# Optimization experiments

Hardware: AMD Instinct MI355X
Metric: run time of the kernel (lower is better)

## Reference

```python
import jax, jax.numpy as jnp
import numpy as np

# dims
B, T, F, R, H = 2048, 50, 64, 6, 64      # batch, time, features, num_rims, hidden per rim
KS, VS = 64, 128                          # input attention key/query size, value size
NC, QC, VC = 4, 32, 16                    # comm heads, comm key/query size, comm value (NC*VC == H)
S = 16                                    # static features
K_ACT = 4                                 # active rims (top-k routing)


def setup_inputs() -> dict:
    key = jax.random.key(0)
    ks = jax.random.split(key, 24)
    f32 = jnp.float32
    rn = lambda k, shape, scale: jax.random.normal(k, shape, f32) * scale
    inp = {}
    inp['x'] = jax.random.normal(ks[0], (B, T, F), f32)
    inp['statics'] = jax.random.normal(ks[1], (B, S), f32)
    inp['mask'] = (jax.random.uniform(ks[2], (B, T, F)) > 0.3).astype(f32)
    inp['delta'] = jax.random.uniform(ks[3], (B, T, F), f32) * 5.0
    inp['x_last_observed'] = jax.random.normal(ks[4], (B, T, F), f32)
    inp['x_mean'] = jax.random.normal(ks[5], (B, F), f32)
    # GRU-D style per-feature input decay params
    inp['w_dg'] = rn(ks[6], (F,), 0.1)
    inp['b_dg'] = jnp.zeros((F,), f32)
    # input attention (shared K/V over the 2-slot [input, null] axis; per-rim group query)
    inp['Wk'] = rn(ks[7], (F, KS), 1.0 / np.sqrt(F))
    inp['Wv'] = rn(ks[8], (F, VS), 1.0 / np.sqrt(F))
    inp['Wq'] = rn(ks[9], (R, H, KS), 1.0 / np.sqrt(H))
    # per-rim (group) GRU cell
    inp['W_ih'] = rn(ks[10], (R, VS, 3 * H), 1.0 / np.sqrt(VS))
    inp['W_hh'] = rn(ks[11], (R, H, 3 * H), 1.0 / np.sqrt(H))
    inp['b_ih'] = jnp.zeros((R, 3 * H), f32)
    inp['b_hh'] = jnp.zeros((R, 3 * H), f32)
    # communication attention (per-rim group projections)
    inp['Wq_c'] = rn(ks[12], (R, H, NC * QC), 1.0 / np.sqrt(H))
    inp['Wk_c'] = rn(ks[13], (R, H, NC * QC), 1.0 / np.sqrt(H))
    inp['Wv_c'] = rn(ks[14], (R, H, NC * VC), 1.0 / np.sqrt(H))
    # MLP head
    inp['W1'] = rn(ks[15], (R * H + S, 10), 1.0 / np.sqrt(R * H + S))
    inp['b1'] = jnp.zeros((10,), f32)
    inp['W2'] = rn(ks[16], (10, 2), 1.0 / np.sqrt(10))
    inp['b2'] = jnp.zeros((2,), f32)
    return inp


def reference(x, statics, mask, delta, x_last_observed, x_mean,
              w_dg, b_dg, Wk, Wv, Wq, W_ih, W_hh, b_ih, b_hh,
              Wq_c, Wk_c, Wv_c, W1, b1, W2, b2):
    Bn = x.shape[0]
    inv_sk = 1.0 / np.sqrt(KS).astype(np.float32)
    inv_sq = 1.0 / np.sqrt(QC).astype(np.float32)

    def step(h, inp_t):
        xt, mt, dt, xlt = inp_t  # each [B,F]
        # GRU-D input decay / imputation
        gamma = jnp.exp(-jax.nn.relu(dt * w_dg + b_dg))
        xh = mt * xt + (1.0 - mt) * (gamma * xlt + (1.0 - gamma) * x_mean)
        # input attention over [real, null] slots
        x_in = jnp.stack([xh, jnp.zeros_like(xh)], axis=1)          # [B,2,F]
        Km = x_in @ Wk                                               # [B,2,KS]
        Vm = x_in @ Wv                                               # [B,2,VS]
        Q = jnp.einsum('brh,rhk->brk', h, Wq)                        # [B,R,KS]
        probs = jax.nn.softmax(jnp.einsum('brk,bnk->brn', Q, Km) * inv_sk, axis=-1)  # [B,R,2]
        inputs = jnp.einsum('brn,bnv->brv', probs, Vm)               # [B,R,VS]
        # top-k active rims = least attention to the null slot
        act_idx = jax.lax.top_k(-probs[:, :, 1], K_ACT)[1]           # [B,K_ACT]
        rim_mask = jnp.sum(jax.nn.one_hot(act_idx, R, dtype=h.dtype), axis=1)  # [B,R]
        # per-rim GRU update (blocked GEMMs)
        gi = jnp.einsum('brv,rvg->brg', inputs, W_ih) + b_ih         # [B,R,3H]
        gh = jnp.einsum('brh,rhg->brg', h, W_hh) + b_hh              # [B,R,3H]
        i_r, i_z, i_n = jnp.split(gi, 3, axis=-1)
        h_r, h_z, h_n = jnp.split(gh, 3, axis=-1)
        r = jax.nn.sigmoid(i_r + h_r)
        z = jax.nn.sigmoid(i_z + h_z)
        n = jnp.tanh(i_n + r * h_n)
        h_new = (1.0 - z) * n + z * h                                # [B,R,H]
        # communication attention among rims
        q = jnp.einsum('brh,rhk->brk', h_new, Wq_c).reshape(Bn, R, NC, QC).transpose(0, 2, 1, 3)
        k = jnp.einsum('brh,rhk->brk', h_new, Wk_c).reshape(Bn, R, NC, QC).transpose(0, 2, 1, 3)
        v = jnp.einsum('brh,rhk->brk', h_new, Wv_c).reshape(Bn, R, NC, VC).transpose(0, 2, 1, 3)
        cprobs = jax.nn.softmax(jnp.einsum('bcrk,bcsk->bcrs', q, k) * inv_sq, axis=-1)  # [B,NC,R,R]
        comm = jnp.einsum('bcrs,bcsv->bcrv', cprobs, v).transpose(0, 2, 1, 3).reshape(Bn, R, NC * VC)
        # only active rims are updated (and receive comm); inactive keep old state
        m = rim_mask[..., None]
        h_out = m * (h_new + comm) + (1.0 - m) * h
        return h_out, None

    h0 = jnp.zeros((Bn, R, H), x.dtype)
    seq = (x.transpose(1, 0, 2), mask.transpose(1, 0, 2),
           delta.transpose(1, 0, 2), x_last_observed.transpose(1, 0, 2))
    hT, _ = jax.lax.scan(step, h0, seq)
    full = jnp.concatenate([hT.reshape(Bn, R * H), statics], axis=1)
    predictions = jax.nn.relu(full @ W1 + b1) @ W2 + b2              # [B,2]
    return predictions
```

## Files before the change

### kernel.cpp

```cpp
#include <hip/hip_runtime.h>
#include <math.h>

#define B_TOT 2048
#define T_STEPS 50
#define F_DIM 64
#define R_RIMS 6
#define H_DIM 64
#define K_ACT 4
#define BB 8

__device__ __forceinline__ void fma4(float4& a, const float4 v, const float s) {
  a.x = fmaf(v.x, s, a.x); a.y = fmaf(v.y, s, a.y);
  a.z = fmaf(v.z, s, a.z); a.w = fmaf(v.w, s, a.w);
}
__device__ __forceinline__ float sigmoidf_(float x) { return 1.0f / (1.0f + __expf(-x)); }
__device__ __forceinline__ float tanhf_(float x) {
  float ax = fabsf(x);
  float e = __expf(-2.0f * ax);
  float t = (1.0f - e) / (1.0f + e);
  return copysignf(t, x);
}

__global__ void wcomb_kernel(const float* __restrict__ Wv, const float* __restrict__ Wih,
                             float* __restrict__ Wc) {
  int g = threadIdx.x;
  int f = blockIdx.x & 63;
  int r = blockIdx.x >> 6;
  float acc = 0.f;
#pragma unroll 8
  for (int v = 0; v < 128; ++v)
    acc = fmaf(Wv[f * 128 + v], Wih[(r * 128 + v) * 192 + g], acc);
  Wc[(r * 64 + f) * 192 + g] = acc;
}

__global__ __launch_bounds__(512, 1) void rims_kernel(
    const float* __restrict__ x, const float* __restrict__ statics,
    const float* __restrict__ maskp, const float* __restrict__ delta,
    const float* __restrict__ xlast, const float* __restrict__ xmean,
    const float* __restrict__ wdgp, const float* __restrict__ bdgp,
    const float* __restrict__ Wk, const float* __restrict__ Wq,
    const float* __restrict__ Whh, const float* __restrict__ bih,
    const float* __restrict__ bhh, const float* __restrict__ Wqc,
    const float* __restrict__ Wkc, const float* __restrict__ Wvc,
    const float* __restrict__ W1, const float* __restrict__ b1,
    const float* __restrict__ W2, const float* __restrict__ b2,
    const float* __restrict__ Wcomb, float* __restrict__ out) {
  __shared__ float xh_T[64][8];
  __shared__ float h_T[6][64][8];
  __shared__ float hn_T[6][64][8];
  __shared__ float K0_T[64][9];
  __shared__ float Q_T[6][64][9];
  __shared__ float qc_T[6][128][9];
  __shared__ float kc_T[6][128][9];
  __shared__ float vc_T[6][64][9];
  __shared__ float bih_l[6 * 192];
  __shared__ float bhh_l[6 * 192];
  __shared__ float p0_l[8][6];
  __shared__ float act_l[8][6];

  const int tid = threadIdx.x;
  const int wave = tid >> 6;
  const int lane = tid & 63;
  const int b0 = blockIdx.x * BB;

  for (int i = tid; i < 6 * 192; i += 512) { bih_l[i] = bih[i]; bhh_l[i] = bhh[i]; }
  for (int i = tid; i < 6 * 64 * 8; i += 512) (&h_T[0][0][0])[i] = 0.f;

  const float wdg = wdgp[lane];
  const float bdg = bdgp[lane];
  const float xmv = xmean[(size_t)(b0 + wave) * 64 + lane];
  __syncthreads();

  for (int t = 0; t < T_STEPS; ++t) {
    {
      size_t off = ((size_t)(b0 + wave) * T_STEPS + t) * 64 + lane;
      float xt = x[off], mt = maskp[off], dt = delta[off], xl = xlast[off];
      float gm = __expf(-fmaxf(fmaf(dt, wdg, bdg), 0.f));
      xh_T[lane][wave] = mt * xt + (1.f - mt) * (gm * xl + (1.f - gm) * xmv);
    }
    __syncthreads();
    if (wave < 7) {
      const float* Ws = (wave == 0) ? Wk : (Wq + (wave - 1) * 64 * 64);
      const float(*src)[8] = (wave == 0) ? xh_T : h_T[wave - 1];
      float4 aL = {0, 0, 0, 0}, aH = {0, 0, 0, 0};
#pragma unroll 8
      for (int l2 = 0; l2 < 64; ++l2) {
        float w = Ws[l2 * 64 + lane];
        float4 sa = *(const float4*)&src[l2][0];
        float4 sb = *(const float4*)&src[l2][4];
        fma4(aL, sa, w); fma4(aH, sb, w);
      }
      float* dst = (wave == 0) ? &K0_T[lane][0] : &Q_T[wave - 1][lane][0];
      dst[0] = aL.x; dst[1] = aL.y; dst[2] = aL.z; dst[3] = aL.w;
      dst[4] = aH.x; dst[5] = aH.y; dst[6] = aH.z; dst[7] = aH.w;
    }
    __syncthreads();
    {
      float k0 = K0_T[lane][wave];
      float logit[6];
#pragma unroll
      for (int r = 0; r < 6; ++r) {
        float p = Q_T[r][lane][wave] * k0;
#pragma unroll
        for (int d = 1; d < 64; d <<= 1) p += __shfl_xor(p, d, 64);
        logit[r] = p * 0.125f;
      }
      if (lane == 0) {
#pragma unroll
        for (int r = 0; r < 6; ++r) {
          int rank = 0;
#pragma unroll
          for (int r2 = 0; r2 < 6; ++r2)
            rank += (logit[r2] > logit[r]) || (logit[r2] == logit[r] && r2 < r);
          p0_l[wave][r] = sigmoidf_(logit[r]);
          act_l[wave][r] = (rank < K_ACT) ? 1.f : 0.f;
        }
      }
    }
    __syncthreads();
    if (wave < 6) {
      const int r = wave;
      const float* Wc = Wcomb + r * 64 * 192;
      const float* Wh = Whh + r * 64 * 192;
      float4 uaL = {0,0,0,0}, uaH = {0,0,0,0}, ubL = {0,0,0,0}, ubH = {0,0,0,0},
             ucL = {0,0,0,0}, ucH = {0,0,0,0};
      float4 gaL = {0,0,0,0}, gaH = {0,0,0,0}, gbL = {0,0,0,0}, gbH = {0,0,0,0},
             gcL = {0,0,0,0}, gcH = {0,0,0,0};
#pragma unroll 4
      for (int l2 = 0; l2 < 64; ++l2) {
        const float* wr = Wc + l2 * 192 + lane;
        float w0 = wr[0], w1 = wr[64], w2 = wr[128];
        const float* vr = Wh + l2 * 192 + lane;
        float v0 = vr[0], v1 = vr[64], v2 = vr[128];
        float4 xa = *(const float4*)&xh_T[l2][0];
        float4 xb = *(const float4*)&xh_T[l2][4];
        float4 ha = *(const float4*)&h_T[r][l2][0];
        float4 hb = *(const float4*)&h_T[r][l2][4];
        fma4(uaL, xa, w0); fma4(uaH, xb, w0);
        fma4(ubL, xa, w1); fma4(ubH, xb, w1);
        fma4(ucL, xa, w2); fma4(ucH, xb, w2);
        fma4(gaL, ha, v0); fma4(gaH, hb, v0);
        fma4(gbL, ha, v1); fma4(gbH, hb, v1);
        fma4(gcL, ha, v2); fma4(gcH, hb, v2);
      }
      const float bir = bih_l[r * 192 + lane], biz = bih_l[r * 192 + 64 + lane],
                  bin = bih_l[r * 192 + 128 + lane];
      const float bhr = bhh_l[r * 192 + lane], bhz = bhh_l[r * 192 + 64 + lane],
                  bhn = bhh_l[r * 192 + 128 + lane];
      float4 holdL = *(const float4*)&h_T[r][lane][0];
      float4 holdH = *(const float4*)&h_T[r][lane][4];
      auto gru1 = [&](float p0v, float u0, float u1, float u2, float g0, float g1,
                      float g2, float hold) -> float {
        float rg = sigmoidf_(fmaf(p0v, u0, bir) + g0 + bhr);
        float zg = sigmoidf_(fmaf(p0v, u1, biz) + g1 + bhz);
        float ng = tanhf_(fmaf(p0v, u2, bin) + rg * (g2 + bhn));
        return (1.f - zg) * ng + zg * hold;
      };
      float4 hnL, hnH;
      hnL.x = gru1(p0_l[0][r], uaL.x, ubL.x, ucL.x, gaL.x, gbL.x, gcL.x, holdL.x);
      hnL.y = gru1(p0_l[1][r], uaL.y, ubL.y, ucL.y, gaL.y, gbL.y, gcL.y, holdL.y);
      hnL.z = gru1(p0_l[2][r], uaL.z, ubL.z, ucL.z, gaL.z, gbL.z, gcL.z, holdL.z);
      hnL.w = gru1(p0_l[3][r], uaL.w, ubL.w, ucL.w, gaL.w, gbL.w, gcL.w, holdL.w);
      hnH.x = gru1(p0_l[4][r], uaH.x, ubH.x, ucH.x, gaH.x, gbH.x, gcH.x, holdH.x);
      hnH.y = gru1(p0_l[5][r], uaH.y, ubH.y, ucH.y, gaH.y, gbH.y, gcH.y, holdH.y);
      hnH.z = gru1(p0_l[6][r], uaH.z, ubH.z, ucH.z, gaH.z, gbH.z, gcH.z, holdH.z);
      hnH.w = gru1(p0_l[7][r], uaH.w, ubH.w, ucH.w, gaH.w, gbH.w, gcH.w, holdH.w);
      *(float4*)&hn_T[r][lane][0] = hnL;
      *(float4*)&hn_T[r][lane][4] = hnH;
    }
    __syncthreads();
    for (int uu = wave; uu < 15; uu += 8) {
      if (uu < 12) {
        const int r = (uu < 6) ? uu : (uu - 6);
        const float* Ws = ((uu < 6) ? Wqc : Wkc) + r * 64 * 128;
        float4 a0L = {0,0,0,0}, a0H = {0,0,0,0}, a1L = {0,0,0,0}, a1H = {0,0,0,0};
#pragma unroll 4
        for (int l2 = 0; l2 < 64; ++l2) {
          float w0 = Ws[l2 * 128 + lane], w1 = Ws[l2 * 128 + 64 + lane];
          float4 ha = *(const float4*)&hn_T[r][l2][0];
          float4 hb = *(const float4*)&hn_T[r][l2][4];
          fma4(a0L, ha, w0); fma4(a0H, hb, w0);
          fma4(a1L, ha, w1); fma4(a1H, hb, w1);
        }
        float(*dst)[9] = (uu < 6) ? qc_T[r] : kc_T[r];
        float* d0 = &dst[lane][0];
        d0[0] = a0L.x; d0[1] = a0L.y; d0[2] = a0L.z; d0[3] = a0L.w;
        d0[4] = a0H.x; d0[5] = a0H.y; d0[6] = a0H.z; d0[7] = a0H.w;
        float* d1 = &dst[lane + 64][0];
        d1[0] = a1L.x; d1[1] = a1L.y; d1[2] = a1L.z; d1[3] = a1L.w;
        d1[4] = a1H.x; d1[5] = a1H.y; d1[6] = a1H.z; d1[7] = a1H.w;
      } else {
        const int rA = (uu - 12) * 2, rB = rA + 1;
        float4 a0L = {0,0,0,0}, a0H = {0,0,0,0}, a1L = {0,0,0,0}, a1H = {0,0,0,0};
#pragma unroll 4
        for (int l2 = 0; l2 < 64; ++l2) {
          float w0 = Wvc[(rA * 64 + l2) * 64 + lane];
          float w1 = Wvc[(rB * 64 + l2) * 64 + lane];
          float4 ha = *(const float4*)&hn_T[rA][l2][0];
          float4 hb = *(const float4*)&hn_T[rA][l2][4];
          float4 hc = *(const float4*)&hn_T[rB][l2][0];
          float4 hd = *(const float4*)&hn_T[rB][l2][4];
          fma4(a0L, ha, w0); fma4(a0H, hb, w0);
          fma4(a1L, hc, w1); fma4(a1H, hd, w1);
        }
        float* d0 = &vc_T[rA][lane][0];
        d0[0] = a0L.x; d0[1] = a0L.y; d0[2] = a0L.z; d0[3] = a0L.w;
        d0[4] = a0H.x; d0[5] = a0H.y; d0[6] = a0H.z; d0[7] = a0H.w;
        float* d1 = &vc_T[rB][lane][0];
        d1[0] = a1L.x; d1[1] = a1L.y; d1[2] = a1L.z; d1[3] = a1L.w;
        d1[4] = a1H.x; d1[5] = a1H.y; d1[6] = a1H.z; d1[7] = a1H.w;
      }
    }
    __syncthreads();
    {
      const int bb = wave;
      float qcA[6], qcB[6], kcA[6], kcB[6], vcv[6];
#pragma unroll
      for (int rr = 0; rr < 6; ++rr) {
        qcA[rr] = qc_T[rr][lane][bb]; qcB[rr] = qc_T[rr][lane + 64][bb];
        kcA[rr] = kc_T[rr][lane][bb]; kcB[rr] = kc_T[rr][lane + 64][bb];
        vcv[rr] = vc_T[rr][lane][bb];
      }
      const int cOut = lane >> 4;
      const int srcLane = (cOut & 1) << 5;
      const float inv_sq = 0.17677669529663687f;
#pragma unroll
      for (int rr = 0; rr < 6; ++rr) {
        float sL[6], sH[6];
#pragma unroll
        for (int s = 0; s < 6; ++s) {
          float p = qcA[rr] * kcA[s];
          p += __shfl_xor(p, 1, 64); p += __shfl_xor(p, 2, 64); p += __shfl_xor(p, 4, 64);
          p += __shfl_xor(p, 8, 64); p += __shfl_xor(p, 16, 64);
          sL[s] = p * inv_sq;
          float q = qcB[rr] * kcB[s];
          q += __shfl_xor(q, 1, 64); q += __shfl_xor(q, 2, 64); q += __shfl_xor(q, 4, 64);
          q += __shfl_xor(q, 8, 64); q += __shfl_xor(q, 16, 64);
          sH[s] = q * inv_sq;
        }
        float mL = sL[0], mH = sH[0];
#pragma unroll
        for (int s = 1; s < 6; ++s) { mL = fmaxf(mL, sL[s]); mH = fmaxf(mH, sH[s]); }
        float sumL = 0.f, sumH = 0.f;
#pragma unroll
        for (int s = 0; s < 6; ++s) {
          sL[s] = __expf(sL[s] - mL); sumL += sL[s];
          sH[s] = __expf(sH[s] - mH); sumH += sH[s];
        }
        float rLn = 1.f / sumL, rHn = 1.f / sumH;
        float comm = 0.f;
#pragma unroll
        for (int s = 0; s < 6; ++s) {
          float tL = __shfl(sL[s] * rLn, srcLane, 64);
          float tH = __shfl(sH[s] * rHn, srcLane, 64);
          float cp = (cOut < 2) ? tL : tH;
          comm = fmaf(cp, vcv[s], comm);
        }
        float mk = act_l[bb][rr];
        float hnv = hn_T[rr][lane][bb];
        float hov = h_T[rr][lane][bb];
        h_T[rr][lane][bb] = (mk > 0.5f) ? (hnv + comm) : hov;
      }
    }
    __syncthreads();
  }

  {
    const int b = b0 + wave;
    float acc[10];
#pragma unroll
    for (int o = 0; o < 10; ++o) acc[o] = 0.f;
#pragma unroll
    for (int ii = 0; ii < 6; ++ii) {
      float f = h_T[ii][lane][wave];
      const float* w = W1 + (ii * 64 + lane) * 10;
#pragma unroll
      for (int o = 0; o < 10; ++o) acc[o] = fmaf(f, w[o], acc[o]);
    }
    if (lane < 16) {
      float f = statics[(size_t)b * 16 + lane];
      const float* w = W1 + (384 + lane) * 10;
#pragma unroll
      for (int o = 0; o < 10; ++o) acc[o] = fmaf(f, w[o], acc[o]);
    }
#pragma unroll
    for (int o = 0; o < 10; ++o) {
#pragma unroll
      for (int d = 1; d < 64; d <<= 1) acc[o] += __shfl_xor(acc[o], d, 64);
    }
    if (lane == 0) {
      float o0 = b2[0], o1 = b2[1];
#pragma unroll
      for (int o = 0; o < 10; ++o) {
        float a = fmaxf(acc[o] + b1[o], 0.f);
        o0 = fmaf(a, W2[o * 2 + 0], o0);
        o1 = fmaf(a, W2[o * 2 + 1], o1);
      }
      out[(size_t)b * 2 + 0] = o0;
      out[(size_t)b * 2 + 1] = o1;
    }
  }
}

extern "C" void kernel_launch(void* const* d_in, const int* in_sizes, int n_in,
                              void* d_out, int out_size, void* d_ws, size_t ws_size,
                              hipStream_t stream) {
  const float* x       = (const float*)d_in[0];
  const float* statics = (const float*)d_in[1];
  const float* maskp   = (const float*)d_in[2];
  const float* delta   = (const float*)d_in[3];
  const float* xlast   = (const float*)d_in[4];
  const float* xmean   = (const float*)d_in[5];
  const float* wdg     = (const float*)d_in[6];
  const float* bdg     = (const float*)d_in[7];
  const float* Wk      = (const float*)d_in[8];
  const float* Wv      = (const float*)d_in[9];
  const float* Wq      = (const float*)d_in[10];
  const float* Wih     = (const float*)d_in[11];
  const float* Whh     = (const float*)d_in[12];
  const float* bih     = (const float*)d_in[13];
  const float* bhh     = (const float*)d_in[14];
  const float* Wqc     = (const float*)d_in[15];
  const float* Wkc     = (const float*)d_in[16];
  const float* Wvc     = (const float*)d_in[17];
  const float* W1      = (const float*)d_in[18];
  const float* b1      = (const float*)d_in[19];
  const float* W2      = (const float*)d_in[20];
  const float* b2      = (const float*)d_in[21];
  float* Wcomb = (float*)d_ws;

  wcomb_kernel<<<384, 192, 0, stream>>>(Wv, Wih, Wcomb);
  rims_kernel<<<256, 512, 0, stream>>>(x, statics, maskp, delta, xlast, xmean,
                                       wdg, bdg, Wk, Wq, Whh, bih, bhh,
                                       Wqc, Wkc, Wvc, W1, b1, W2, b2,
                                       Wcomb, (float*)d_out);
}
```

Measured before the change: 1.737 ms.

## Halve per-block batch, transpose weights for float4 loads, raise occupancy

```diff
diff --git a/kernel.cpp b/kernel.cpp
--- a/kernel.cpp
+++ b/kernel.cpp
@@ -1,13 +1,16 @@
 #include <hip/hip_runtime.h>
 #include <math.h>
 
-#define B_TOT 2048
 #define T_STEPS 50
-#define F_DIM 64
-#define R_RIMS 6
-#define H_DIM 64
-#define K_ACT 4
-#define BB 8
+#define BB 4
+
+#define OFF_WCT   0
+#define OFF_WHHT  73728
+#define OFF_WQT   147456
+#define OFF_WKT   172032
+#define OFF_WQCT  176128
+#define OFF_WKCT  225280
+#define OFF_WVCT  274432
 
 __device__ __forceinline__ void fma4(float4& a, const float4 v, const float s) {
   a.x = fmaf(v.x, s, a.x); a.y = fmaf(v.y, s, a.y);
@@ -21,58 +24,86 @@
   return copysignf(t, x);
 }
 
-__global__ void wcomb_kernel(const float* __restrict__ Wv, const float* __restrict__ Wih,
-                             float* __restrict__ Wc) {
-  int g = threadIdx.x;
-  int f = blockIdx.x & 63;
-  int r = blockIdx.x >> 6;
+__global__ void wcombT_kernel(const float* __restrict__ Wv, const float* __restrict__ Wih,
+                              float* __restrict__ ws) {
+  int f = threadIdx.x;
+  int g = blockIdx.x % 192;
+  int r = blockIdx.x / 192;
   float acc = 0.f;
 #pragma unroll 8
   for (int v = 0; v < 128; ++v)
     acc = fmaf(Wv[f * 128 + v], Wih[(r * 128 + v) * 192 + g], acc);
-  Wc[(r * 64 + f) * 192 + g] = acc;
-}
-
-__global__ __launch_bounds__(512, 1) void rims_kernel(
+  ws[OFF_WCT + (r * 192 + g) * 64 + f] = acc;
+}
+
+__global__ void prep_transpose(const float* __restrict__ Whh, const float* __restrict__ Wq,
+                               const float* __restrict__ Wk, const float* __restrict__ Wqc,
+                               const float* __restrict__ Wkc, const float* __restrict__ Wvc,
+                               float* __restrict__ ws) {
+  int i = blockIdx.x * 256 + threadIdx.x;
+  if (i < 73728) {
+    int r = i / 12288, rem = i % 12288, g = rem / 64, h2 = rem % 64;
+    ws[OFF_WHHT + i] = Whh[(r * 64 + h2) * 192 + g];
+  } else if (i < 98304) {
+    int j = i - 73728;
+    int r = j / 4096, rem = j % 4096, k = rem / 64, h2 = rem % 64;
+    ws[OFF_WQT + j] = Wq[(r * 64 + h2) * 64 + k];
+  } else if (i < 102400) {
+    int j = i - 98304;
+    int k = j / 64, f = j % 64;
+    ws[OFF_WKT + j] = Wk[f * 64 + k];
+  } else if (i < 151552) {
+    int j = i - 102400;
+    int r = j / 8192, rem = j % 8192, g = rem / 64, h2 = rem % 64;
+    ws[OFF_WQCT + j] = Wqc[(r * 64 + h2) * 128 + g];
+  } else if (i < 200704) {
+    int j = i - 151552;
+    int r = j / 8192, rem = j % 8192, g = rem / 64, h2 = rem % 64;
+    ws[OFF_WKCT + j] = Wkc[(r * 64 + h2) * 128 + g];
+  } else if (i < 225280) {
+    int j = i - 200704;
+    int r = j / 4096, rem = j % 4096, g = rem / 64, h2 = rem % 64;
+    ws[OFF_WVCT + j] = Wvc[(r * 64 + h2) * 64 + g];
+  }
+}
+
+__global__ __launch_bounds__(512, 4) void rims_kernel(
     const float* __restrict__ x, const float* __restrict__ statics,
     const float* __restrict__ maskp, const float* __restrict__ delta,
     const float* __restrict__ xlast, const float* __restrict__ xmean,
     const float* __restrict__ wdgp, const float* __restrict__ bdgp,
-    const float* __restrict__ Wk, const float* __restrict__ Wq,
-    const float* __restrict__ Whh, const float* __restrict__ bih,
-    const float* __restrict__ bhh, const float* __restrict__ Wqc,
-    const float* __restrict__ Wkc, const float* __restrict__ Wvc,
+    const float* __restrict__ bih, const float* __restrict__ bhh,
     const float* __restrict__ W1, const float* __restrict__ b1,
     const float* __restrict__ W2, const float* __restrict__ b2,
-    const float* __restrict__ Wcomb, float* __restrict__ out) {
-  __shared__ float xh_T[64][8];
-  __shared__ float h_T[6][64][8];
-  __shared__ float hn_T[6][64][8];
-  __shared__ float K0_T[64][9];
-  __shared__ float Q_T[6][64][9];
-  __shared__ float qc_T[6][128][9];
-  __shared__ float kc_T[6][128][9];
-  __shared__ float vc_T[6][64][9];
-  __shared__ float bih_l[6 * 192];
-  __shared__ float bhh_l[6 * 192];
-  __shared__ float p0_l[8][6];
-  __shared__ float act_l[8][6];
+    const float* __restrict__ ws, float* __restrict__ out) {
+  __shared__ float xh_T[64][4];
+  __shared__ float h_T[6][64][4];
+  __shared__ float hn_T[6][64][4];
+  __shared__ float K0_R[4][64];
+  __shared__ float Q_R[6][4][64];
+  __shared__ float qc_R[6][4][128];
+  __shared__ float kc_R[6][4][128];
+  __shared__ float vc_R[6][4][64];
+  __shared__ float bih_l[1152];
+  __shared__ float bhh_l[1152];
+  __shared__ float p0_l[4][6];
+  __shared__ float act_l[4][6];
 
   const int tid = threadIdx.x;
   const int wave = tid >> 6;
   const int lane = tid & 63;
   const int b0 = blockIdx.x * BB;
 
-  for (int i = tid; i < 6 * 192; i += 512) { bih_l[i] = bih[i]; bhh_l[i] = bhh[i]; }
-  for (int i = tid; i < 6 * 64 * 8; i += 512) (&h_T[0][0][0])[i] = 0.f;
+  for (int i = tid; i < 1152; i += 512) { bih_l[i] = bih[i]; bhh_l[i] = bhh[i]; }
+  for (int i = tid; i < 6 * 64 * 4; i += 512) (&h_T[0][0][0])[i] = 0.f;
 
   const float wdg = wdgp[lane];
   const float bdg = bdgp[lane];
-  const float xmv = xmean[(size_t)(b0 + wave) * 64 + lane];
+  const float xmv = xmean[(size_t)(b0 + (wave & 3)) * 64 + lane];
   __syncthreads();
 
   for (int t = 0; t < T_STEPS; ++t) {
-    {
+    if (wave < 4) {
       size_t off = ((size_t)(b0 + wave) * T_STEPS + t) * 64 + lane;
       float xt = x[off], mt = maskp[off], dt = delta[off], xl = xlast[off];
       float gm = __expf(-fmaxf(fmaf(dt, wdg, bdg), 0.f));
@@ -80,27 +111,34 @@
     }
     __syncthreads();
     if (wave < 7) {
-      const float* Ws = (wave == 0) ? Wk : (Wq + (wave - 1) * 64 * 64);
-      const float(*src)[8] = (wave == 0) ? xh_T : h_T[wave - 1];
-      float4 aL = {0, 0, 0, 0}, aH = {0, 0, 0, 0};
-#pragma unroll 8
-      for (int l2 = 0; l2 < 64; ++l2) {
-        float w = Ws[l2 * 64 + lane];
-        float4 sa = *(const float4*)&src[l2][0];
-        float4 sb = *(const float4*)&src[l2][4];
-        fma4(aL, sa, w); fma4(aH, sb, w);
-      }
-      float* dst = (wave == 0) ? &K0_T[lane][0] : &Q_T[wave - 1][lane][0];
-      dst[0] = aL.x; dst[1] = aL.y; dst[2] = aL.z; dst[3] = aL.w;
-      dst[4] = aH.x; dst[5] = aH.y; dst[6] = aH.z; dst[7] = aH.w;
-    }
-    __syncthreads();
-    {
-      float k0 = K0_T[lane][wave];
+      const float* WT = (wave == 0) ? (ws + OFF_WKT) : (ws + OFF_WQT + (wave - 1) * 4096);
+      const float(*srcT)[4] = (wave == 0) ? xh_T : h_T[wave - 1];
+      float4 acc = {0, 0, 0, 0};
+#pragma unroll 4
+      for (int kk = 0; kk < 16; ++kk) {
+        float4 wv = *(const float4*)(WT + lane * 64 + kk * 4);
+        float4 a0 = *(const float4*)&srcT[kk * 4 + 0][0];
+        float4 a1 = *(const float4*)&srcT[kk * 4 + 1][0];
+        float4 a2 = *(const float4*)&srcT[kk * 4 + 2][0];
+        float4 a3 = *(const float4*)&srcT[kk * 4 + 3][0];
+        fma4(acc, a0, wv.x); fma4(acc, a1, wv.y); fma4(acc, a2, wv.z); fma4(acc, a3, wv.w);
+      }
+      if (wave == 0) {
+        K0_R[0][lane] = acc.x; K0_R[1][lane] = acc.y;
+        K0_R[2][lane] = acc.z; K0_R[3][lane] = acc.w;
+      } else {
+        float* q = &Q_R[wave - 1][0][0];
+        q[lane] = acc.x; q[64 + lane] = acc.y; q[128 + lane] = acc.z; q[192 + lane] = acc.w;
+      }
+    }
+    __syncthreads();
+    if (wave < 4) {
+      const int bb = wave;
+      float k0 = K0_R[bb][lane];
       float logit[6];
 #pragma unroll
       for (int r = 0; r < 6; ++r) {
-        float p = Q_T[r][lane][wave] * k0;
+        float p = Q_R[r][bb][lane] * k0;
 #pragma unroll
         for (int d = 1; d < 64; d <<= 1) p += __shfl_xor(p, d, 64);
         logit[r] = p * 0.125f;
@@ -112,128 +150,130 @@
 #pragma unroll
           for (int r2 = 0; r2 < 6; ++r2)
             rank += (logit[r2] > logit[r]) || (logit[r2] == logit[r] && r2 < r);
-          p0_l[wave][r] = sigmoidf_(logit[r]);
-          act_l[wave][r] = (rank < K_ACT) ? 1.f : 0.f;
+          p0_l[bb][r] = sigmoidf_(logit[r]);
+          act_l[bb][r] = (rank < 4) ? 1.f : 0.f;
         }
       }
     }
     __syncthreads();
     if (wave < 6) {
       const int r = wave;
-      const float* Wc = Wcomb + r * 64 * 192;
-      const float* Wh = Whh + r * 64 * 192;
-      float4 uaL = {0,0,0,0}, uaH = {0,0,0,0}, ubL = {0,0,0,0}, ubH = {0,0,0,0},
-             ucL = {0,0,0,0}, ucH = {0,0,0,0};
-      float4 gaL = {0,0,0,0}, gaH = {0,0,0,0}, gbL = {0,0,0,0}, gbH = {0,0,0,0},
-             gcL = {0,0,0,0}, gcH = {0,0,0,0};
-#pragma unroll 4
-      for (int l2 = 0; l2 < 64; ++l2) {
-        const float* wr = Wc + l2 * 192 + lane;
-        float w0 = wr[0], w1 = wr[64], w2 = wr[128];
-        const float* vr = Wh + l2 * 192 + lane;
-        float v0 = vr[0], v1 = vr[64], v2 = vr[128];
-        float4 xa = *(const float4*)&xh_T[l2][0];
-        float4 xb = *(const float4*)&xh_T[l2][4];
-        float4 ha = *(const float4*)&h_T[r][l2][0];
-        float4 hb = *(const float4*)&h_T[r][l2][4];
-        fma4(uaL, xa, w0); fma4(uaH, xb, w0);
-        fma4(ubL, xa, w1); fma4(ubH, xb, w1);
-        fma4(ucL, xa, w2); fma4(ucH, xb, w2);
-        fma4(gaL, ha, v0); fma4(gaH, hb, v0);
-        fma4(gbL, ha, v1); fma4(gbH, hb, v1);
-        fma4(gcL, ha, v2); fma4(gcH, hb, v2);
+      const float* WcT = ws + OFF_WCT + r * 12288;
+      const float* WhT = ws + OFF_WHHT + r * 12288;
+      float4 ua = {0,0,0,0}, ub = {0,0,0,0}, uc = {0,0,0,0};
+      float4 ga = {0,0,0,0}, gb = {0,0,0,0}, gc = {0,0,0,0};
+#pragma unroll 2
+      for (int kk = 0; kk < 16; ++kk) {
+        float4 w0 = *(const float4*)(WcT + lane * 64 + kk * 4);
+        float4 w1 = *(const float4*)(WcT + (lane + 64) * 64 + kk * 4);
+        float4 w2 = *(const float4*)(WcT + (lane + 128) * 64 + kk * 4);
+        float4 v0 = *(const float4*)(WhT + lane * 64 + kk * 4);
+        float4 v1 = *(const float4*)(WhT + (lane + 64) * 64 + kk * 4);
+        float4 v2 = *(const float4*)(WhT + (lane + 128) * 64 + kk * 4);
+#define G1J(J, W0C, W1C, W2C, V0C, V1C, V2C)                      \
+        {                                                          \
+          float4 xv = *(const float4*)&xh_T[kk * 4 + J][0];        \
+          float4 hv = *(const float4*)&h_T[r][kk * 4 + J][0];      \
+          fma4(ua, xv, W0C); fma4(ub, xv, W1C); fma4(uc, xv, W2C); \
+          fma4(ga, hv, V0C); fma4(gb, hv, V1C); fma4(gc, hv, V2C); \
+        }
+        G1J(0, w0.x, w1.x, w2.x, v0.x, v1.x, v2.x)
+        G1J(1, w0.y, w1.y, w2.y, v0.y, v1.y, v2.y)
+        G1J(2, w0.z, w1.z, w2.z, v0.z, v1.z, v2.z)
+        G1J(3, w0.w, w1.w, w2.w, v0.w, v1.w, v2.w)
+#undef G1J
       }
       const float bir = bih_l[r * 192 + lane], biz = bih_l[r * 192 + 64 + lane],
                   bin = bih_l[r * 192 + 128 + lane];
       const float bhr = bhh_l[r * 192 + lane], bhz = bhh_l[r * 192 + 64 + lane],
                   bhn = bhh_l[r * 192 + 128 + lane];
-      float4 holdL = *(const float4*)&h_T[r][lane][0];
-      float4 holdH = *(const float4*)&h_T[r][lane][4];
+      float4 hold = *(const float4*)&h_T[r][lane][0];
       auto gru1 = [&](float p0v, float u0, float u1, float u2, float g0, float g1,
-                      float g2, float hold) -> float {
+                      float g2, float holdv) -> float {
         float rg = sigmoidf_(fmaf(p0v, u0, bir) + g0 + bhr);
         float zg = sigmoidf_(fmaf(p0v, u1, biz) + g1 + bhz);
         float ng = tanhf_(fmaf(p0v, u2, bin) + rg * (g2 + bhn));
-        return (1.f - zg) * ng + zg * hold;
+        return (1.f - zg) * ng + zg * holdv;
       };
-      float4 hnL, hnH;
-      hnL.x = gru1(p0_l[0][r], uaL.x, ubL.x, ucL.x, gaL.x, gbL.x, gcL.x, holdL.x);
-      hnL.y = gru1(p0_l[1][r], uaL.y, ubL.y, ucL.y, gaL.y, gbL.y, gcL.y, holdL.y);
-      hnL.z = gru1(p0_l[2][r], uaL.z, ubL.z, ucL.z, gaL.z, gbL.z, gcL.z, holdL.z);
-      hnL.w = gru1(p0_l[3][r], uaL.w, ubL.w, ucL.w, gaL.w, gbL.w, gcL.w, holdL.w);
-      hnH.x = gru1(p0_l[4][r], uaH.x, ubH.x, ucH.x, gaH.x, gbH.x, gcH.x, holdH.x);
-      hnH.y = gru1(p0_l[5][r], uaH.y, ubH.y, ucH.y, gaH.y, gbH.y, gcH.y, holdH.y);
-      hnH.z = gru1(p0_l[6][r], uaH.z, ubH.z, ucH.z, gaH.z, gbH.z, gcH.z, holdH.z);
-      hnH.w = gru1(p0_l[7][r], uaH.w, ubH.w, ucH.w, gaH.w, gbH.w, gcH.w, holdH.w);
-      *(float4*)&hn_T[r][lane][0] = hnL;
-      *(float4*)&hn_T[r][lane][4] = hnH;
+      float4 hn;
+      hn.x = gru1(p0_l[0][r], ua.x, ub.x, uc.x, ga.x, gb.x, gc.x, hold.x);
+      hn.y = gru1(p0_l[1][r], ua.y, ub.y, uc.y, ga.y, gb.y, gc.y, hold.y);
+      hn.z = gru1(p0_l[2][r], ua.z, ub.z, uc.z, ga.z, gb.z, gc.z, hold.z);
+      hn.w = gru1(p0_l[3][r], ua.w, ub.w, uc.w, ga.w, gb.w, gc.w, hold.w);
+      *(float4*)&hn_T[r][lane][0] = hn;
     }
     __syncthreads();
     for (int uu = wave; uu < 15; uu += 8) {
       if (uu < 12) {
         const int r = (uu < 6) ? uu : (uu - 6);
-        const float* Ws = ((uu < 6) ? Wqc : Wkc) + r * 64 * 128;
-        float4 a0L = {0,0,0,0}, a0H = {0,0,0,0}, a1L = {0,0,0,0}, a1H = {0,0,0,0};
+        const float* WT = ws + ((uu < 6) ? OFF_WQCT : OFF_WKCT) + r * 8192;
+        float4 a0 = {0,0,0,0}, a1 = {0,0,0,0};
 #pragma unroll 4
-        for (int l2 = 0; l2 < 64; ++l2) {
-          float w0 = Ws[l2 * 128 + lane], w1 = Ws[l2 * 128 + 64 + lane];
-          float4 ha = *(const float4*)&hn_T[r][l2][0];
-          float4 hb = *(const float4*)&hn_T[r][l2][4];
-          fma4(a0L, ha, w0); fma4(a0H, hb, w0);
-          fma4(a1L, ha, w1); fma4(a1H, hb, w1);
-        }
-        float(*dst)[9] = (uu < 6) ? qc_T[r] : kc_T[r];
-        float* d0 = &dst[lane][0];
-        d0[0] = a0L.x; d0[1] = a0L.y; d0[2] = a0L.z; d0[3] = a0L.w;
-        d0[4] = a0H.x; d0[5] = a0H.y; d0[6] = a0H.z; d0[7] = a0H.w;
-        float* d1 = &dst[lane + 64][0];
-        d1[0] = a1L.x; d1[1] = a1L.y; d1[2] = a1L.z; d1[3] = a1L.w;
-        d1[4] = a1H.x; d1[5] = a1H.y; d1[6] = a1H.z; d1[7] = a1H.w;
+        for (int kk = 0; kk < 16; ++kk) {
+          float4 w0 = *(const float4*)(WT + lane * 64 + kk * 4);
+          float4 w1 = *(const float4*)(WT + (lane + 64) * 64 + kk * 4);
+#define C1J(J, W0C, W1C)                                      \
+          {                                                    \
+            float4 xv = *(const float4*)&hn_T[r][kk * 4 + J][0]; \
+            fma4(a0, xv, W0C); fma4(a1, xv, W1C);              \
+          }
+          C1J(0, w0.x, w1.x) C1J(1, w0.y, w1.y) C1J(2, w0.z, w1.z) C1J(3, w0.w, w1.w)
+#undef C1J
+        }
+        float* dst = (uu < 6) ? &qc_R[r][0][0] : &kc_R[r][0][0];
+        dst[0 * 128 + lane] = a0.x; dst[1 * 128 + lane] = a0.y;
+        dst[2 * 128 + lane] = a0.z; dst[3 * 128 + lane] = a0.w;
+        dst[0 * 128 + 64 + lane] = a1.x; dst[1 * 128 + 64 + lane] = a1.y;
+        dst[2 * 128 + 64 + lane] = a1.z; dst[3 * 128 + 64 + lane] = a1.w;
       } else {
         const int rA = (uu - 12) * 2, rB = rA + 1;
-        float4 a0L = {0,0,0,0}, a0H = {0,0,0,0}, a1L = {0,0,0,0}, a1H = {0,0,0,0};
+        const float* WT = ws + OFF_WVCT;
+        float4 a0 = {0,0,0,0}, a1 = {0,0,0,0};
 #pragma unroll 4
-        for (int l2 = 0; l2 < 64; ++l2) {
-          float w0 = Wvc[(rA * 64 + l2) * 64 + lane];
-          float w1 = Wvc[(rB * 64 + l2) * 64 + lane];
-          float4 ha = *(const float4*)&hn_T[rA][l2][0];
-          float4 hb = *(const float4*)&hn_T[rA][l2][4];
-          float4 hc = *(const float4*)&hn_T[rB][l2][0];
-          float4 hd = *(const float4*)&hn_T[rB][l2][4];
-          fma4(a0L, ha, w0); fma4(a0H, hb, w0);
-          fma4(a1L, hc, w1); fma4(a1H, hd, w1);
-        }
-        float* d0 = &vc_T[rA][lane][0];
-        d0[0] = a0L.x; d0[1] = a0L.y; d0[2] = a0L.z; d0[3] = a0L.w;
-        d0[4] = a0H.x; d0[5] = a0H.y; d0[6] = a0H.z; d0[7] = a0H.w;
-        float* d1 = &vc_T[rB][lane][0];
-        d1[0] = a1L.x; d1[1] = a1L.y; d1[2] = a1L.z; d1[3] = a1L.w;
-        d1[4] = a1H.x; d1[5] = a1H.y; d1[6] = a1H.z; d1[7] = a1H.w;
+        for (int kk = 0; kk < 16; ++kk) {
+          float4 w0 = *(const float4*)(WT + (rA * 64 + lane) * 64 + kk * 4);
+          float4 w1 = *(const float4*)(WT + (rB * 64 + lane) * 64 + kk * 4);
+#define C1V(J, W0C, W1C)                                        \
+          {                                                      \
+            float4 xa = *(const float4*)&hn_T[rA][kk * 4 + J][0]; \
+            float4 xb = *(const float4*)&hn_T[rB][kk * 4 + J][0]; \
+            fma4(a0, xa, W0C); fma4(a1, xb, W1C);                \
+          }
+          C1V(0, w0.x, w1.x) C1V(1, w0.y, w1.y) C1V(2, w0.z, w1.z) C1V(3, w0.w, w1.w)
+#undef C1V
+        }
+        vc_R[rA][0][lane] = a0.x; vc_R[rA][1][lane] = a0.y;
+        vc_R[rA][2][lane] = a0.z; vc_R[rA][3][lane] = a0.w;
+        vc_R[rB][0][lane] = a1.x; vc_R[rB][1][lane] = a1.y;
+        vc_R[rB][2][lane] = a1.z; vc_R[rB][3][lane] = a1.w;
       }
     }
     __syncthreads();
     {
-      const int bb = wave;
-      float qcA[6], qcB[6], kcA[6], kcB[6], vcv[6];
-#pragma unroll
-      for (int rr = 0; rr < 6; ++rr) {
-        qcA[rr] = qc_T[rr][lane][bb]; qcB[rr] = qc_T[rr][lane + 64][bb];
-        kcA[rr] = kc_T[rr][lane][bb]; kcB[rr] = kc_T[rr][lane + 64][bb];
-        vcv[rr] = vc_T[rr][lane][bb];
+      const int bb = wave >> 1;
+      const int half = wave & 1;
+      float kcA[6], kcB[6], vcv[6];
+#pragma unroll
+      for (int s = 0; s < 6; ++s) {
+        kcA[s] = kc_R[s][bb][lane];
+        kcB[s] = kc_R[s][bb][64 + lane];
+        vcv[s] = vc_R[s][bb][lane];
       }
       const int cOut = lane >> 4;
       const int srcLane = (cOut & 1) << 5;
       const float inv_sq = 0.17677669529663687f;
 #pragma unroll
-      for (int rr = 0; rr < 6; ++rr) {
+      for (int jr = 0; jr < 3; ++jr) {
+        const int rr = half * 3 + jr;
+        float qA = qc_R[rr][bb][lane], qB = qc_R[rr][bb][64 + lane];
         float sL[6], sH[6];
 #pragma unroll
         for (int s = 0; s < 6; ++s) {
-          float p = qcA[rr] * kcA[s];
+          float p = qA * kcA[s];
           p += __shfl_xor(p, 1, 64); p += __shfl_xor(p, 2, 64); p += __shfl_xor(p, 4, 64);
           p += __shfl_xor(p, 8, 64); p += __shfl_xor(p, 16, 64);
           sL[s] = p * inv_sq;
-          float q = qcB[rr] * kcB[s];
+          float q = qB * kcB[s];
           q += __shfl_xor(q, 1, 64); q += __shfl_xor(q, 2, 64); q += __shfl_xor(q, 4, 64);
           q += __shfl_xor(q, 8, 64); q += __shfl_xor(q, 16, 64);
           sH[s] = q * inv_sq;
@@ -265,7 +305,7 @@
     __syncthreads();
   }
 
-  {
+  if (wave < 4) {
     const int b = b0 + wave;
     float acc[10];
 #pragma unroll
@@ -327,11 +367,11 @@
   const float* b1      = (const float*)d_in[19];
   const float* W2      = (const float*)d_in[20];
   const float* b2      = (const float*)d_in[21];
-  float* Wcomb = (float*)d_ws;
-
-  wcomb_kernel<<<384, 192, 0, stream>>>(Wv, Wih, Wcomb);
-  rims_kernel<<<256, 512, 0, stream>>>(x, statics, maskp, delta, xlast, xmean,
-                                       wdg, bdg, Wk, Wq, Whh, bih, bhh,
-                                       Wqc, Wkc, Wvc, W1, b1, W2, b2,
-                                       Wcomb, (float*)d_out);
-}
+  float* ws = (float*)d_ws;
+
+  wcombT_kernel<<<1152, 64, 0, stream>>>(Wv, Wih, ws);
+  prep_transpose<<<880, 256, 0, stream>>>(Whh, Wq, Wk, Wqc, Wkc, Wvc, ws);
+  rims_kernel<<<512, 512, 0, stream>>>(x, statics, maskp, delta, xlast, xmean,
+                                       wdg, bdg, bih, bhh, W1, b1, W2, b2,
+                                       ws, (float*)d_out);
+}
```

After: 4.036 ms. +132.4%, slower.

## Double block to 1024 threads, splitting batch rows across wave pairs per stage

Applied to the files above, without the earlier changes.

```diff
diff --git a/kernel.cpp b/kernel.cpp
--- a/kernel.cpp
+++ b/kernel.cpp
@@ -1,12 +1,7 @@
 #include <hip/hip_runtime.h>
 #include <math.h>
 
-#define B_TOT 2048
 #define T_STEPS 50
-#define F_DIM 64
-#define R_RIMS 6
-#define H_DIM 64
-#define K_ACT 4
 #define BB 8
 
 __device__ __forceinline__ void fma4(float4& a, const float4 v, const float s) {
@@ -33,7 +28,7 @@
   Wc[(r * 64 + f) * 192 + g] = acc;
 }
 
-__global__ __launch_bounds__(512, 1) void rims_kernel(
+__global__ __launch_bounds__(1024, 1) void rims_kernel(
     const float* __restrict__ x, const float* __restrict__ statics,
     const float* __restrict__ maskp, const float* __restrict__ delta,
     const float* __restrict__ xlast, const float* __restrict__ xmean,
@@ -48,13 +43,11 @@
   __shared__ float xh_T[64][8];
   __shared__ float h_T[6][64][8];
   __shared__ float hn_T[6][64][8];
-  __shared__ float K0_T[64][9];
-  __shared__ float Q_T[6][64][9];
-  __shared__ float qc_T[6][128][9];
-  __shared__ float kc_T[6][128][9];
-  __shared__ float vc_T[6][64][9];
-  __shared__ float bih_l[6 * 192];
-  __shared__ float bhh_l[6 * 192];
+  __shared__ float K0_R[8][64];
+  __shared__ float Q_R[6][8][64];
+  __shared__ float qc_R[6][8][128];
+  __shared__ float kc_R[6][8][128];
+  __shared__ float vc_R[6][8][64];
   __shared__ float p0_l[8][6];
   __shared__ float act_l[8][6];
 
@@ -63,44 +56,57 @@
   const int lane = tid & 63;
   const int b0 = blockIdx.x * BB;
 
-  for (int i = tid; i < 6 * 192; i += 512) { bih_l[i] = bih[i]; bhh_l[i] = bhh[i]; }
-  for (int i = tid; i < 6 * 64 * 8; i += 512) (&h_T[0][0][0])[i] = 0.f;
+  for (int i = tid; i < 6 * 64 * 8; i += 1024) (&h_T[0][0][0])[i] = 0.f;
 
   const float wdg = wdgp[lane];
   const float bdg = bdgp[lane];
-  const float xmv = xmean[(size_t)(b0 + wave) * 64 + lane];
+  const float xmv = xmean[(size_t)(b0 + (wave & 7)) * 64 + lane];
+  float bir = 0.f, biz = 0.f, bin = 0.f, bhr = 0.f, bhz = 0.f, bhn = 0.f;
+  if (wave < 12) {
+    const int r = wave >> 1;
+    bir = bih[r * 192 + lane]; biz = bih[r * 192 + 64 + lane];
+    bin = bih[r * 192 + 128 + lane];
+    bhr = bhh[r * 192 + lane]; bhz = bhh[r * 192 + 64 + lane];
+    bhn = bhh[r * 192 + 128 + lane];
+  }
   __syncthreads();
 
   for (int t = 0; t < T_STEPS; ++t) {
-    {
+    if (wave < 8) {
       size_t off = ((size_t)(b0 + wave) * T_STEPS + t) * 64 + lane;
       float xt = x[off], mt = maskp[off], dt = delta[off], xl = xlast[off];
       float gm = __expf(-fmaxf(fmaf(dt, wdg, bdg), 0.f));
       xh_T[lane][wave] = mt * xt + (1.f - mt) * (gm * xl + (1.f - gm) * xmv);
     }
     __syncthreads();
-    if (wave < 7) {
-      const float* Ws = (wave == 0) ? Wk : (Wq + (wave - 1) * 64 * 64);
-      const float(*src)[8] = (wave == 0) ? xh_T : h_T[wave - 1];
-      float4 aL = {0, 0, 0, 0}, aH = {0, 0, 0, 0};
+    if (wave < 14) {
+      const int p = wave >> 1, q = wave & 1;
+      const float* W = (p == 0) ? Wk : (Wq + (p - 1) * 4096);
+      const float(*src)[8] = (p == 0) ? xh_T : h_T[p - 1];
+      float4 acc = {0, 0, 0, 0};
 #pragma unroll 8
-      for (int l2 = 0; l2 < 64; ++l2) {
-        float w = Ws[l2 * 64 + lane];
-        float4 sa = *(const float4*)&src[l2][0];
-        float4 sb = *(const float4*)&src[l2][4];
-        fma4(aL, sa, w); fma4(aH, sb, w);
-      }
-      float* dst = (wave == 0) ? &K0_T[lane][0] : &Q_T[wave - 1][lane][0];
-      dst[0] = aL.x; dst[1] = aL.y; dst[2] = aL.z; dst[3] = aL.w;
-      dst[4] = aH.x; dst[5] = aH.y; dst[6] = aH.z; dst[7] = aH.w;
-    }
-    __syncthreads();
-    {
-      float k0 = K0_T[lane][wave];
+      for (int k = 0; k < 64; ++k) {
+        float w = W[k * 64 + lane];
+        float4 a = *(const float4*)&src[k][q * 4];
+        fma4(acc, a, w);
+      }
+      if (p == 0) {
+        K0_R[q * 4 + 0][lane] = acc.x; K0_R[q * 4 + 1][lane] = acc.y;
+        K0_R[q * 4 + 2][lane] = acc.z; K0_R[q * 4 + 3][lane] = acc.w;
+      } else {
+        float(*Qr)[64] = Q_R[p - 1];
+        Qr[q * 4 + 0][lane] = acc.x; Qr[q * 4 + 1][lane] = acc.y;
+        Qr[q * 4 + 2][lane] = acc.z; Qr[q * 4 + 3][lane] = acc.w;
+      }
+    }
+    __syncthreads();
+    if (wave < 8) {
+      const int row = wave;
+      float k0 = K0_R[row][lane];
       float logit[6];
 #pragma unroll
       for (int r = 0; r < 6; ++r) {
-        float p = Q_T[r][lane][wave] * k0;
+        float p = Q_R[r][row][lane] * k0;
 #pragma unroll
         for (int d = 1; d < 64; d <<= 1) p += __shfl_xor(p, d, 64);
         logit[r] = p * 0.125f;
@@ -112,128 +118,103 @@
 #pragma unroll
           for (int r2 = 0; r2 < 6; ++r2)
             rank += (logit[r2] > logit[r]) || (logit[r2] == logit[r] && r2 < r);
-          p0_l[wave][r] = sigmoidf_(logit[r]);
-          act_l[wave][r] = (rank < K_ACT) ? 1.f : 0.f;
-        }
-      }
-    }
-    __syncthreads();
-    if (wave < 6) {
-      const int r = wave;
-      const float* Wc = Wcomb + r * 64 * 192;
-      const float* Wh = Whh + r * 64 * 192;
-      float4 uaL = {0,0,0,0}, uaH = {0,0,0,0}, ubL = {0,0,0,0}, ubH = {0,0,0,0},
-             ucL = {0,0,0,0}, ucH = {0,0,0,0};
-      float4 gaL = {0,0,0,0}, gaH = {0,0,0,0}, gbL = {0,0,0,0}, gbH = {0,0,0,0},
-             gcL = {0,0,0,0}, gcH = {0,0,0,0};
+          p0_l[row][r] = sigmoidf_(logit[r]);
+          act_l[row][r] = (rank < 4) ? 1.f : 0.f;
+        }
+      }
+    }
+    __syncthreads();
+    if (wave < 12) {
+      const int r = wave >> 1, q = wave & 1;
+      const float* Wc = Wcomb + r * 12288;
+      const float* Wh = Whh + r * 12288;
+      float4 ur = {0,0,0,0}, uz = {0,0,0,0}, un = {0,0,0,0};
+      float4 gr = {0,0,0,0}, gz = {0,0,0,0}, gn = {0,0,0,0};
 #pragma unroll 4
-      for (int l2 = 0; l2 < 64; ++l2) {
-        const float* wr = Wc + l2 * 192 + lane;
-        float w0 = wr[0], w1 = wr[64], w2 = wr[128];
-        const float* vr = Wh + l2 * 192 + lane;
-        float v0 = vr[0], v1 = vr[64], v2 = vr[128];
-        float4 xa = *(const float4*)&xh_T[l2][0];
-        float4 xb = *(const float4*)&xh_T[l2][4];
-        float4 ha = *(const float4*)&h_T[r][l2][0];
-        float4 hb = *(const float4*)&h_T[r][l2][4];
-        fma4(uaL, xa, w0); fma4(uaH, xb, w0);
-        fma4(ubL, xa, w1); fma4(ubH, xb, w1);
-        fma4(ucL, xa, w2); fma4(ucH, xb, w2);
-        fma4(gaL, ha, v0); fma4(gaH, hb, v0);
-        fma4(gbL, ha, v1); fma4(gbH, hb, v1);
-        fma4(gcL, ha, v2); fma4(gcH, hb, v2);
-      }
-      const float bir = bih_l[r * 192 + lane], biz = bih_l[r * 192 + 64 + lane],
-                  bin = bih_l[r * 192 + 128 + lane];
-      const float bhr = bhh_l[r * 192 + lane], bhz = bhh_l[r * 192 + 64 + lane],
-                  bhn = bhh_l[r * 192 + 128 + lane];
-      float4 holdL = *(const float4*)&h_T[r][lane][0];
-      float4 holdH = *(const float4*)&h_T[r][lane][4];
+      for (int k = 0; k < 64; ++k) {
+        float w0 = Wc[k * 192 + lane], w1 = Wc[k * 192 + 64 + lane],
+              w2 = Wc[k * 192 + 128 + lane];
+        float v0 = Wh[k * 192 + lane], v1 = Wh[k * 192 + 64 + lane],
+              v2 = Wh[k * 192 + 128 + lane];
+        float4 xv = *(const float4*)&xh_T[k][q * 4];
+        float4 hv = *(const float4*)&h_T[r][k][q * 4];
+        fma4(ur, xv, w0); fma4(uz, xv, w1); fma4(un, xv, w2);
+        fma4(gr, hv, v0); fma4(gz, hv, v1); fma4(gn, hv, v2);
+      }
+      float4 hold = *(const float4*)&h_T[r][lane][q * 4];
       auto gru1 = [&](float p0v, float u0, float u1, float u2, float g0, float g1,
-                      float g2, float hold) -> float {
+                      float g2, float holdv) -> float {
         float rg = sigmoidf_(fmaf(p0v, u0, bir) + g0 + bhr);
         float zg = sigmoidf_(fmaf(p0v, u1, biz) + g1 + bhz);
         float ng = tanhf_(fmaf(p0v, u2, bin) + rg * (g2 + bhn));
-        return (1.f - zg) * ng + zg * hold;
+        return (1.f - zg) * ng + zg * holdv;
       };
-      float4 hnL, hnH;
-      hnL.x = gru1(p0_l[0][r], uaL.x, ubL.x, ucL.x, gaL.x, gbL.x, gcL.x, holdL.x);
-      hnL.y = gru1(p0_l[1][r], uaL.y, ubL.y, ucL.y, gaL.y, gbL.y, gcL.y, holdL.y);
-      hnL.z = gru1(p0_l[2][r], uaL.z, ubL.z, ucL.z, gaL.z, gbL.z, gcL.z, holdL.z);
-      hnL.w = gru1(p0_l[3][r], uaL.w, ubL.w, ucL.w, gaL.w, gbL.w, gcL.w, holdL.w);
-      hnH.x = gru1(p0_l[4][r], uaH.x, ubH.x, ucH.x, gaH.x, gbH.x, gcH.x, holdH.x);
-      hnH.y = gru1(p0_l[5][r], uaH.y, ubH.y, ucH.y, gaH.y, gbH.y, gcH.y, holdH.y);
-      hnH.z = gru1(p0_l[6][r], uaH.z, ubH.z, ucH.z, gaH.z, gbH.z, gcH.z, holdH.z);
-      hnH.w = gru1(p0_l[7][r], uaH.w, ubH.w, ucH.w, gaH.w, gbH.w, gcH.w, holdH.w);
-      *(float4*)&hn_T[r][lane][0] = hnL;
-      *(float4*)&hn_T[r][lane][4] = hnH;
-    }
-    __syncthreads();
-    for (int uu = wave; uu < 15; uu += 8) {
-      if (uu < 12) {
-        const int r = (uu < 6) ? uu : (uu - 6);
-        const float* Ws = ((uu < 6) ? Wqc : Wkc) + r * 64 * 128;
-        float4 a0L = {0,0,0,0}, a0H = {0,0,0,0}, a1L = {0,0,0,0}, a1H = {0,0,0,0};
+      float4 hn;
+      hn.x = gru1(p0_l[q * 4 + 0][r], ur.x, uz.x, un.x, gr.x, gz.x, gn.x, hold.x);
+      hn.y = gru1(p0_l[q * 4 + 1][r], ur.y, uz.y, un.y, gr.y, gz.y, gn.y, hold.y);
+      hn.z = gru1(p0_l[q * 4 + 2][r], ur.z, uz.z, un.z, gr.z, gz.z, gn.z, hold.z);
+      hn.w = gru1(p0_l[q * 4 + 3][r], ur.w, uz.w, un.w, gr.w, gz.w, gn.w, hold.w);
+      *(float4*)&hn_T[r][lane][q * 4] = hn;
+    }
+    __syncthreads();
+    for (int u = wave; u < 36; u += 16) {
+      if (u < 24) {
+        const int v = (u < 12) ? u : (u - 12);
+        const int r = v >> 1, q = v & 1;
+        const float* W = ((u < 12) ? Wqc : Wkc) + r * 8192;
+        float4 a0 = {0,0,0,0}, a1 = {0,0,0,0};
 #pragma unroll 4
-        for (int l2 = 0; l2 < 64; ++l2) {
-          float w0 = Ws[l2 * 128 + lane], w1 = Ws[l2 * 128 + 64 + lane];
-          float4 ha = *(const float4*)&hn_T[r][l2][0];
-          float4 hb = *(const float4*)&hn_T[r][l2][4];
-          fma4(a0L, ha, w0); fma4(a0H, hb, w0);
-          fma4(a1L, ha, w1); fma4(a1H, hb, w1);
-        }
-        float(*dst)[9] = (uu < 6) ? qc_T[r] : kc_T[r];
-        float* d0 = &dst[lane][0];
-        d0[0] = a0L.x; d0[1] = a0L.y; d0[2] = a0L.z; d0[3] = a0L.w;
-        d0[4] = a0H.x; d0[5] = a0H.y; d0[6] = a0H.z; d0[7] = a0H.w;
-        float* d1 = &dst[lane + 64][0];
-        d1[0] = a1L.x; d1[1] = a1L.y; d1[2] = a1L.z; d1[3] = a1L.w;
-        d1[4] = a1H.x; d1[5] = a1H.y; d1[6] = a1H.z; d1[7] = a1H.w;
+        for (int k = 0; k < 64; ++k) {
+          float w0 = W[k * 128 + lane], w1 = W[k * 128 + 64 + lane];
+          float4 a = *(const float4*)&hn_T[r][k][q * 4];
+          fma4(a0, a, w0); fma4(a1, a, w1);
+        }
+        float(*dst)[128] = (u < 12) ? qc_R[r] : kc_R[r];
+        dst[q * 4 + 0][lane] = a0.x; dst[q * 4 + 1][lane] = a0.y;
+        dst[q * 4 + 2][lane] = a0.z; dst[q * 4 + 3][lane] = a0.w;
+        dst[q * 4 + 0][64 + lane] = a1.x; dst[q * 4 + 1][64 + lane] = a1.y;
+        dst[q * 4 + 2][64 + lane] = a1.z; dst[q * 4 + 3][64 + lane] = a1.w;
       } else {
-        const int rA = (uu - 12) * 2, rB = rA + 1;
-        float4 a0L = {0,0,0,0}, a0H = {0,0,0,0}, a1L = {0,0,0,0}, a1H = {0,0,0,0};
+        const int v = u - 24;
+        const int r = v >> 1, q = v & 1;
+        const float* W = Wvc + r * 4096;
+        float4 a0 = {0,0,0,0};
 #pragma unroll 4
-        for (int l2 = 0; l2 < 64; ++l2) {
-          float w0 = Wvc[(rA * 64 + l2) * 64 + lane];
-          float w1 = Wvc[(rB * 64 + l2) * 64 + lane];
-          float4 ha = *(const float4*)&hn_T[rA][l2][0];
-          float4 hb = *(const float4*)&hn_T[rA][l2][4];
-          float4 hc = *(const float4*)&hn_T[rB][l2][0];
-          float4 hd = *(const float4*)&hn_T[rB][l2][4];
-          fma4(a0L, ha, w0); fma4(a0H, hb, w0);
-          fma4(a1L, hc, w1); fma4(a1H, hd, w1);
-        }
-        float* d0 = &vc_T[rA][lane][0];
-        d0[0] = a0L.x; d0[1] = a0L.y; d0[2] = a0L.z; d0[3] = a0L.w;
-        d0[4] = a0H.x; d0[5] = a0H.y; d0[6] = a0H.z; d0[7] = a0H.w;
-        float* d1 = &vc_T[rB][lane][0];
-        d1[0] = a1L.x; d1[1] = a1L.y; d1[2] = a1L.z; d1[3] = a1L.w;
-        d1[4] = a1H.x; d1[5] = a1H.y; d1[6] = a1H.z; d1[7] = a1H.w;
+        for (int k = 0; k < 64; ++k) {
+          float w = W[k * 64 + lane];
+          float4 a = *(const float4*)&hn_T[r][k][q * 4];
+          fma4(a0, a, w);
+        }
+        vc_R[r][q * 4 + 0][lane] = a0.x; vc_R[r][q * 4 + 1][lane] = a0.y;
+        vc_R[r][q * 4 + 2][lane] = a0.z; vc_R[r][q * 4 + 3][lane] = a0.w;
       }
     }
     __syncthreads();
     {
-      const int bb = wave;
-      float qcA[6], qcB[6], kcA[6], kcB[6], vcv[6];
-#pragma unroll
-      for (int rr = 0; rr < 6; ++rr) {
-        qcA[rr] = qc_T[rr][lane][bb]; qcB[rr] = qc_T[rr][lane + 64][bb];
-        kcA[rr] = kc_T[rr][lane][bb]; kcB[rr] = kc_T[rr][lane + 64][bb];
-        vcv[rr] = vc_T[rr][lane][bb];
+      const int row = wave >> 1;
+      const int half = wave & 1;
+      float kcA[6], kcB[6], vcv[6];
+#pragma unroll
+      for (int s = 0; s < 6; ++s) {
+        kcA[s] = kc_R[s][row][lane];
+        kcB[s] = kc_R[s][row][64 + lane];
+        vcv[s] = vc_R[s][row][lane];
       }
       const int cOut = lane >> 4;
       const int srcLane = (cOut & 1) << 5;
       const float inv_sq = 0.17677669529663687f;
 #pragma unroll
-      for (int rr = 0; rr < 6; ++rr) {
+      for (int jr = 0; jr < 3; ++jr) {
+        const int rr = half * 3 + jr;
+        float qA = qc_R[rr][row][lane], qB = qc_R[rr][row][64 + lane];
         float sL[6], sH[6];
 #pragma unroll
         for (int s = 0; s < 6; ++s) {
-          float p = qcA[rr] * kcA[s];
+          float p = qA * kcA[s];
           p += __shfl_xor(p, 1, 64); p += __shfl_xor(p, 2, 64); p += __shfl_xor(p, 4, 64);
           p += __shfl_xor(p, 8, 64); p += __shfl_xor(p, 16, 64);
           sL[s] = p * inv_sq;
-          float q = qcB[rr] * kcB[s];
+          float q = qB * kcB[s];
           q += __shfl_xor(q, 1, 64); q += __shfl_xor(q, 2, 64); q += __shfl_xor(q, 4, 64);
           q += __shfl_xor(q, 8, 64); q += __shfl_xor(q, 16, 64);
           sH[s] = q * inv_sq;
@@ -256,16 +237,16 @@
           float cp = (cOut < 2) ? tL : tH;
           comm = fmaf(cp, vcv[s], comm);
         }
-        float mk = act_l[bb][rr];
-        float hnv = hn_T[rr][lane][bb];
-        float hov = h_T[rr][lane][bb];
-        h_T[rr][lane][bb] = (mk > 0.5f) ? (hnv + comm) : hov;
+        float mk = act_l[row][rr];
+        float hnv = hn_T[rr][lane][row];
+        float hov = h_T[rr][lane][row];
+        h_T[rr][lane][row] = (mk > 0.5f) ? (hnv + comm) : hov;
       }
     }
     __syncthreads();
   }
 
-  {
+  if (wave < 8) {
     const int b = b0 + wave;
     float acc[10];
 #pragma unroll
@@ -330,8 +311,8 @@
   float* Wcomb = (float*)d_ws;
 
   wcomb_kernel<<<384, 192, 0, stream>>>(Wv, Wih, Wcomb);
-  rims_kernel<<<256, 512, 0, stream>>>(x, statics, maskp, delta, xlast, xmean,
-                                       wdg, bdg, Wk, Wq, Whh, bih, bhh,
-                                       Wqc, Wkc, Wvc, W1, b1, W2, b2,
-                                       Wcomb, (float*)d_out);
-}
+  rims_kernel<<<256, 1024, 0, stream>>>(x, statics, maskp, delta, xlast, xmean,
+                                        wdg, bdg, Wk, Wq, Whh, bih, bhh,
+                                        Wqc, Wkc, Wvc, W1, b1, W2, b2,
+                                        Wcomb, (float*)d_out);
+}
```

Result: faster. 1.692 ms (-2.6%).
